# Kernel optimization log

Hardware: AMD Instinct MI355X
Metric: run time of the kernel (lower is better)

Reference implementation:

```python
import jax, jax.numpy as jnp
import numpy as np


def _conv_relu(x, w, b):
    # keras Conv2D: NHWC input, HWIO kernel, VALID padding, stride 1, relu
    y = jax.lax.conv_general_dilated(
        x, w, window_strides=(1, 1), padding='VALID',
        dimension_numbers=('NHWC', 'HWIO', 'NHWC'))
    return jax.nn.relu(y + b)


def _maxpool2(x):
    # keras MaxPooling2D((2,2)): window 2x2, stride 2, VALID
    return jax.lax.reduce_window(
        x, -jnp.inf, jax.lax.max,
        window_dimensions=(1, 2, 2, 1), window_strides=(1, 2, 2, 1),
        padding='VALID')


def setup_inputs() -> dict:
    key = jax.random.key(0)
    ks = jax.random.split(key, 8)
    B = 4096
    return {
        'x': jax.random.normal(ks[0], (B, 14, 14, 1), jnp.float32),
        'conv1_w': jax.random.normal(ks[1], (3, 3, 1, 32), jnp.float32) * 0.1,
        'conv1_b': jnp.zeros((32,), jnp.float32),
        'conv2_w': jax.random.normal(ks[2], (3, 3, 32, 64), jnp.float32) * 0.05,
        'conv2_b': jnp.zeros((64,), jnp.float32),
        # trainable grid, initialized as tf.linspace(0,1,grid_size=50)
        'grid': jnp.linspace(0.0, 1.0, 50, dtype=jnp.float32),
        # KANLayer splines: output_dim=128 weights, each (input_dim=256, grid_size=50)
        'kan1_w': jax.random.normal(ks[3], (128, 256, 50), jnp.float32) * 0.05,
        # SimplifiedKANLayer splines: output_dim=64 weights, each (input_dim=128,)
        'kan2_w': jax.random.normal(ks[4], (64, 128), jnp.float32) * 0.05,
        'dense_w': jax.random.normal(ks[5], (64, 10), jnp.float32) * 0.05,
        'dense_b': jnp.zeros((10,), jnp.float32),
    }


def reference(x, conv1_w, conv1_b, conv2_w, conv2_b, grid, kan1_w, kan2_w,
              dense_w, dense_b):
    h = _conv_relu(x, conv1_w, conv1_b)   # (B,12,12,32)
    h = _maxpool2(h)                      # (B,6,6,32)
    h = _conv_relu(h, conv2_w, conv2_b)   # (B,4,4,64)
    h = _maxpool2(h)                      # (B,2,2,64)
    B = h.shape[0]
    h = h.reshape(B, -1)                  # (B,256) keras Flatten order (H,W,C)
    # KANLayer: linear hat basis relu(1-|x-g|) per (feature,grid), contracted
    # against per-output coefficients: out[b,o] = sum_{d,g} W[o,d,g]*basis[b,d,g]
    basis = jax.nn.relu(1.0 - jnp.abs(h[:, :, None] - grid[None, None, :]))  # (B,256,50)
    h = jnp.einsum('bdg,odg->bo', basis, kan1_w)  # (B,128)
    # SimplifiedKANLayer: out[b,o] = sum_d W2[o,d]*relu(h[b,d])
    h = jnp.einsum('bd,od->bo', jax.nn.relu(h), kan2_w)  # (B,64)
    return jax.nn.softmax(h @ dense_w + dense_b, axis=-1)  # (B,10)
```

## Files before the change

### kernel.cpp

```cpp
#include <hip/hip_runtime.h>
#include <hip/hip_bf16.h>
#include <hip/hip_fp16.h>

typedef float v2f __attribute__((ext_vector_type(2)));
typedef _Float16 f16x8 __attribute__((ext_vector_type(8)));
typedef float f32x4 __attribute__((ext_vector_type(4)));

#define NBC 4

__global__ __launch_bounds__(256) void k_prep(
    const float* __restrict__ kan1_w, const float* __restrict__ w2,
    const float* __restrict__ kan2_w, __half* __restrict__ tabN,
    _Float16* __restrict__ w2f, __half2* __restrict__ w2t) {
  __shared__ float wsh[128][51];
  int bid = blockIdx.x;
  int t = threadIdx.x;
  if (bid < 1024) {
    int d = bid >> 2;
    int q = bid & 3;
#pragma unroll
    for (int i = t; i < 128 * 50; i += 256) {
      int oo = i / 50;
      int g = i - oo * 50;
      wsh[oo][g] = kan1_w[(size_t)oo * 12800 + (size_t)d * 50 + g];
    }
    __syncthreads();
    int o = t & 127;
    int jh = t >> 7;
    const float* wr = &wsh[o][0];
    __half* trow = tabN + (size_t)d * 197 * 128 + o;
    const float inv98 = 1.0f / 98.0f;
    int ci = q * 2 + jh;
    int k0 = (ci * 98) >> 3;
    int k1 = ((ci + 1) * 98) >> 3;
    float lowW = 0.f, lowG = 0.f, highW = 0.f, highG = 0.f;
    {
      int gl0 = k0 - 48 > 0 ? k0 - 48 : 0;
      int gl1 = k0 < 49 ? k0 : 49;
      for (int g = gl0; g <= gl1; ++g) {
        float w = wr[g], gg = (float)g * (1.0f / 49.0f);
        lowW += w; lowG += w * gg;
      }
      for (int g = k0 + 1; g < 50; ++g) {
        float w = wr[g], gg = (float)g * (1.0f / 49.0f);
        highW += w; highG += w * gg;
      }
    }
    for (int k = k0; k < k1; ++k) {
      float A = highW - lowW;
      float Bc = (lowW + highW) + lowG - highG;
      float c0 = (float)(2 * k) * inv98 + 0.5f * inv98;
      float c1 = c0 + inv98;
      trow[(size_t)(2 * k) * 128] = __float2half(fmaf(A, c0, Bc));
      trow[(size_t)(2 * k + 1) * 128] = __float2half(fmaf(A, c1, Bc));
      if (k + 1 <= 49) {
        float wg = wr[k + 1], gg = (float)(k + 1) * (1.0f / 49.0f);
        lowW += wg; lowG += wg * gg;
        highW -= wg; highG -= wg * gg;
      }
      if (k >= 48) {
        float wg = wr[k - 48], gg = (float)(k - 48) * (1.0f / 49.0f);
        lowW -= wg; lowG -= wg * gg;
      }
    }
    if (ci == 7) trow[(size_t)196 * 128] = __float2half(0.f);
    return;
  }
  if (bid < 1096) {
    int i = (bid - 1024) * 256 + t;
    int n = i & 63;
    int row = i >> 6;
    int ci = row & 31;
    int tap = row >> 5;
    w2f[((tap * 4 + (ci >> 3)) * 64 + n) * 8 + (ci & 7)] = (_Float16)w2[i];
    return;
  }
  {
    int i = (bid - 1096) * 256 + t;
    int dp = i >> 6;
    int o = i & 63;
    w2t[i] = __floats2half2_rn(kan2_w[o * 128 + 2 * dp],
                               kan2_w[o * 128 + 2 * dp + 1]);
  }
}

__global__ __launch_bounds__(256)
__attribute__((amdgpu_waves_per_eu(2, 4))) void k_conv(
    const float* __restrict__ x, const float* __restrict__ w1,
    const float* __restrict__ b1, const _Float16* __restrict__ w2f,
    const float* __restrict__ b2, unsigned short* __restrict__ metaG) {
  __shared__ __align__(16) char sm1[4864];
  __shared__ __align__(16) char sm2[11520];
  float* xs = (float*)sm1;
  float* w1s = xs + NBC * 224;
  float* b1s = w1s + 288;
  _Float16* h1l = (_Float16*)sm2;
  int t = threadIdx.x;
  int bid = blockIdx.x;
  int b0 = bid * NBC;
  {
    for (int i = t; i < NBC * 224; i += 256) {
      int blb = i / 224;
      int rem = i - blb * 224;
      int r = rem >> 4;
      int cc = rem & 15;
      xs[i] = (cc < 14) ? x[(size_t)(b0 + blb) * 196 + r * 14 + cc] : 0.f;
    }
    for (int i = t; i < 288; i += 256) w1s[i] = w1[i];
    if (t < 32) b1s[t] = b1[t];
  }
  __syncthreads();
  int p = t >> 6;
  int c = t & 63;
  {
    int ch = c & 31;
    int half = c >> 5;
    float wr[9];
#pragma unroll
    for (int j = 0; j < 9; ++j) wr[j] = w1s[j * 32 + ch];
    float bias = b1s[ch];
    int y0 = 3 * half;
    const float* xb = xs + p * 224;
    _Float16* hrow = h1l + p * 1440 + ch;
#pragma unroll
    for (int yy = 0; yy < 3; ++yy) {
      int y = y0 + yy;
      float xr[4][16];
#pragma unroll
      for (int r = 0; r < 4; ++r) {
        float4* dstp = (float4*)xr[r];
        const float4* srcp = (const float4*)(xb + (2 * y + r) * 16);
#pragma unroll
        for (int q = 0; q < 4; ++q) dstp[q] = srcp[q];
      }
#pragma unroll
      for (int xx = 0; xx < 6; ++xx) {
        float m = -1e30f;
#pragma unroll
        for (int py = 0; py < 2; ++py)
#pragma unroll
          for (int px = 0; px < 2; ++px) {
            float s = 0.f;
#pragma unroll
            for (int dy = 0; dy < 3; ++dy)
#pragma unroll
              for (int dx = 0; dx < 3; ++dx)
                s = fmaf(xr[py + dy][2 * xx + px + dx], wr[dy * 3 + dx], s);
            m = fmaxf(m, s);
          }
        hrow[(y * 6 + xx) * 40] = (_Float16)fmaxf(m + bias, 0.f);
      }
    }
  }
  __syncthreads();
  {
    int lm = c & 15;
    int lk = c >> 4;
    int mbase = (lm >> 2) * 6 + (lm & 3);
    f32x4 acc[4];
#pragma unroll
    for (int nt = 0; nt < 4; ++nt) acc[nt] = (f32x4){0.f, 0.f, 0.f, 0.f};
    const _Float16* h0 = &h1l[p * 1440 + lk * 8];
#pragma unroll
    for (int tap = 0; tap < 9; ++tap) {
      int tapoff = (tap / 3) * 6 + (tap % 3);
      int po = (mbase + tapoff) * 40;
      f16x8 a0 = *(const f16x8*)(h0 + po);
      const _Float16* wb = &w2f[((tap * 4 + lk) * 64 + lm) * 8];
      f16x8 bf0 = *(const f16x8*)(wb);
      f16x8 bf1 = *(const f16x8*)(wb + 128);
      f16x8 bf2 = *(const f16x8*)(wb + 256);
      f16x8 bf3 = *(const f16x8*)(wb + 384);
      acc[0] = __builtin_amdgcn_mfma_f32_16x16x32_f16(a0, bf0, acc[0], 0, 0, 0);
      acc[1] = __builtin_amdgcn_mfma_f32_16x16x32_f16(a0, bf1, acc[1], 0, 0, 0);
      acc[2] = __builtin_amdgcn_mfma_f32_16x16x32_f16(a0, bf2, acc[2], 0, 0, 0);
      acc[3] = __builtin_amdgcn_mfma_f32_16x16x32_f16(a0, bf3, acc[3], 0, 0, 0);
    }
    float bias[4];
#pragma unroll
    for (int nt = 0; nt < 4; ++nt) bias[nt] = b2[nt * 16 + lm];
#pragma unroll
    for (int nt = 0; nt < 4; ++nt) {
      f32x4 A = acc[nt];
      float m01 = fmaxf(A.x, A.y);
      float m23 = fmaxf(A.z, A.w);
      m01 = fmaxf(m01, __shfl_xor(m01, 16));
      m23 = fmaxf(m23, __shfl_xor(m23, 16));
      float val = (lk & 1) ? m23 : m01;
      val = fmaxf(val + bias[nt], 0.f);
      int d = lk * 64 + nt * 16 + lm;
      int k = (int)(val * 98.0f);
      k = k > 196 ? 196 : k;
      metaG[(size_t)(b0 + p) * 256 + d] = (unsigned short)(d * 197 + k);
    }
  }
}

__global__ __launch_bounds__(256) void k_gather(
    const __half* __restrict__ tabN, const unsigned short* __restrict__ metaG,
    float* __restrict__ partialG, int B) {
  __shared__ unsigned short ms[32][32];
  int bid = blockIdx.x;
  int t = threadIdx.x;
  int s = bid & 7;
  int gid = bid >> 3;
  int b0 = gid * 32;
  {
    unsigned int* mdst = (unsigned int*)&ms[0][0];
    for (int j = t; j < 512; j += 256) {
      int row = j >> 4, col = j & 15;
      mdst[j] = *(const unsigned int*)(metaG + (size_t)(b0 + row) * 256 +
                                       s * 32 + col * 2);
    }
  }
  __syncthreads();
  int w = t >> 6;
  int l = t & 63;
  for (int bb = 0; bb < 8; ++bb) {
    int brow = w * 8 + bb;
    float ax = 0.f, ay = 0.f;
#pragma unroll
    for (int ch = 0; ch < 4; ++ch) {
      __half2 hsum = __builtin_bit_cast(__half2, 0u);
#pragma unroll
      for (int dd = 0; dd < 8; ++dd) {
        int off = ((int)ms[brow][ch * 8 + dd]) << 7;
        hsum = __hadd2(hsum, *(const __half2*)(tabN + off + 2 * l));
      }
      float2 f = __half22float2(hsum);
      ax += f.x;
      ay += f.y;
    }
    *(float2*)(partialG + ((size_t)s * B + (b0 + brow)) * 128 + 2 * l) =
        make_float2(ax, ay);
  }
}

__global__ __launch_bounds__(256) void k_tail(
    const float* __restrict__ partialG, const __half2* __restrict__ w2t,
    const float* __restrict__ dense_w, const float* __restrict__ dense_b,
    float* __restrict__ out, int B) {
  __shared__ float vs[NBC * 128];
  __shared__ float us[NBC * 64];
  __shared__ float ls[NBC * 12];
  int t = threadIdx.x;
  int bid = blockIdx.x;
  int b0 = bid * NBC;
  for (int i = t; i < NBC * 128; i += 256) {
    int bb = i >> 7;
    int o = i & 127;
    float sum = 0.f;
#pragma unroll
    for (int s = 0; s < 8; ++s)
      sum += partialG[((size_t)s * B + (b0 + bb)) * 128 + o];
    vs[i] = fmaxf(sum, 0.f);
  }
  __syncthreads();
  int p = t >> 6;
  int c = t & 63;
  {
    float a = 0.f;
    const float* v0 = vs + p * 128;
#pragma unroll 8
    for (int dp = 0; dp < 64; ++dp) {
      float2 wf = __half22float2(w2t[dp * 64 + c]);
      float2 vq = *(const float2*)(v0 + 2 * dp);
      a = fmaf(wf.x, vq.x, a);
      a = fmaf(wf.y, vq.y, a);
    }
    us[p * 64 + c] = a;
  }
  __syncthreads();
  if (t < NBC * 10) {
    int b = t / 10;
    int j = t - b * 10;
    float s = dense_b[j];
    for (int k2 = 0; k2 < 64; ++k2)
      s = fmaf(us[b * 64 + k2], dense_w[k2 * 10 + j], s);
    ls[b * 12 + j] = s;
  }
  __syncthreads();
  if (t < NBC) {
    int b = t;
    float m = -1e30f;
#pragma unroll
    for (int j = 0; j < 10; ++j) m = fmaxf(m, ls[b * 12 + j]);
    float e[10];
    float sum = 0.f;
#pragma unroll
    for (int j = 0; j < 10; ++j) {
      e[j] = __expf(ls[b * 12 + j] - m);
      sum += e[j];
    }
    float inv = 1.0f / sum;
#pragma unroll
    for (int j = 0; j < 10; ++j) out[(size_t)(b0 + b) * 10 + j] = e[j] * inv;
  }
}

extern "C" void kernel_launch(void* const* d_in, const int* in_sizes, int n_in,
                              void* d_out, int out_size, void* d_ws, size_t ws_size,
                              hipStream_t stream) {
  const float* x      = (const float*)d_in[0];
  const float* w1     = (const float*)d_in[1];
  const float* b1     = (const float*)d_in[2];
  const float* w2     = (const float*)d_in[3];
  const float* b2     = (const float*)d_in[4];
  const float* kan1_w = (const float*)d_in[6];
  const float* kan2_w = (const float*)d_in[7];
  const float* dw     = (const float*)d_in[8];
  const float* db     = (const float*)d_in[9];
  float* out = (float*)d_out;
  int B = in_sizes[0] / 196;

  char* wsb = (char*)d_ws;
  __half* tabN = (__half*)wsb;
  size_t off1 = (size_t)256 * 197 * 128 * sizeof(__half);
  off1 = (off1 + 255) & ~(size_t)255;
  _Float16* w2f = (_Float16*)(wsb + off1);
  size_t off2 = off1 + 18432 * sizeof(_Float16);
  off2 = (off2 + 255) & ~(size_t)255;
  __half2* w2t = (__half2*)(wsb + off2);
  size_t off3 = off2 + 4096 * sizeof(__half2);
  off3 = (off3 + 255) & ~(size_t)255;
  unsigned short* metaG = (unsigned short*)(wsb + off3);
  size_t off4 = off3 + (size_t)B * 256 * sizeof(unsigned short);
  off4 = (off4 + 255) & ~(size_t)255;
  float* partialG = (float*)(wsb + off4);

  k_prep<<<dim3(1112), dim3(256), 0, stream>>>(kan1_w, w2, kan2_w, tabN, w2f, w2t);
  k_conv<<<dim3(B / NBC), dim3(256), 0, stream>>>(x, w1, b1, w2f, b2, metaG);
  k_gather<<<dim3(8 * (B / 32)), dim3(256), 0, stream>>>(tabN, metaG, partialG, B);
  k_tail<<<dim3(B / NBC), dim3(256), 0, stream>>>(partialG, w2t, dw, db, out, B);
}
```

Baseline: 124.4 us.

## Replace KAN1 table-gather with dense MFMA contraction over hat basis

Drops the precomputed piecewise-linear lookup table and gather kernel, and computes the KAN layer as a dense fp16 MFMA GEMM. The hat basis is generated on the fly from conv outputs stored as fp16, against kan1_w repacked to a padded (256x56) K layout. This removes the large table build and the scattered gathers, but adds a roughly 14336-long K reduction per output. The split-K partials also drop from 8 to 4. The prep kernel now only converts weights, and k_kan1 launches 256 blocks with one block per CU.

```diff
diff --git a/kernel.cpp b/kernel.cpp
--- a/kernel.cpp
+++ b/kernel.cpp
@@ -10,64 +10,22 @@
 
 __global__ __launch_bounds__(256) void k_prep(
     const float* __restrict__ kan1_w, const float* __restrict__ w2,
-    const float* __restrict__ kan2_w, __half* __restrict__ tabN,
+    const float* __restrict__ kan2_w, _Float16* __restrict__ w1f,
     _Float16* __restrict__ w2f, __half2* __restrict__ w2t) {
-  __shared__ float wsh[128][51];
   int bid = blockIdx.x;
   int t = threadIdx.x;
-  if (bid < 1024) {
-    int d = bid >> 2;
-    int q = bid & 3;
-#pragma unroll
-    for (int i = t; i < 128 * 50; i += 256) {
-      int oo = i / 50;
-      int g = i - oo * 50;
-      wsh[oo][g] = kan1_w[(size_t)oo * 12800 + (size_t)d * 50 + g];
-    }
-    __syncthreads();
-    int o = t & 127;
-    int jh = t >> 7;
-    const float* wr = &wsh[o][0];
-    __half* trow = tabN + (size_t)d * 197 * 128 + o;
-    const float inv98 = 1.0f / 98.0f;
-    int ci = q * 2 + jh;
-    int k0 = (ci * 98) >> 3;
-    int k1 = ((ci + 1) * 98) >> 3;
-    float lowW = 0.f, lowG = 0.f, highW = 0.f, highG = 0.f;
-    {
-      int gl0 = k0 - 48 > 0 ? k0 - 48 : 0;
-      int gl1 = k0 < 49 ? k0 : 49;
-      for (int g = gl0; g <= gl1; ++g) {
-        float w = wr[g], gg = (float)g * (1.0f / 49.0f);
-        lowW += w; lowG += w * gg;
-      }
-      for (int g = k0 + 1; g < 50; ++g) {
-        float w = wr[g], gg = (float)g * (1.0f / 49.0f);
-        highW += w; highG += w * gg;
-      }
-    }
-    for (int k = k0; k < k1; ++k) {
-      float A = highW - lowW;
-      float Bc = (lowW + highW) + lowG - highG;
-      float c0 = (float)(2 * k) * inv98 + 0.5f * inv98;
-      float c1 = c0 + inv98;
-      trow[(size_t)(2 * k) * 128] = __float2half(fmaf(A, c0, Bc));
-      trow[(size_t)(2 * k + 1) * 128] = __float2half(fmaf(A, c1, Bc));
-      if (k + 1 <= 49) {
-        float wg = wr[k + 1], gg = (float)(k + 1) * (1.0f / 49.0f);
-        lowW += wg; lowG += wg * gg;
-        highW -= wg; highG -= wg * gg;
-      }
-      if (k >= 48) {
-        float wg = wr[k - 48], gg = (float)(k - 48) * (1.0f / 49.0f);
-        lowW -= wg; lowG -= wg * gg;
-      }
-    }
-    if (ci == 7) trow[(size_t)196 * 128] = __float2half(0.f);
+  if (bid < 7168) {
+    int i = bid * 256 + t;
+    int o = i / 14336;
+    int kk = i - o * 14336;
+    int d = kk / 56;
+    int g = kk - d * 56;
+    float val = (g < 50) ? kan1_w[(size_t)o * 12800 + d * 50 + g] : 0.f;
+    w1f[(size_t)(kk >> 3) * 1024 + o * 8 + (kk & 7)] = (_Float16)val;
     return;
   }
-  if (bid < 1096) {
-    int i = (bid - 1024) * 256 + t;
+  if (bid < 7240) {
+    int i = (bid - 7168) * 256 + t;
     int n = i & 63;
     int row = i >> 6;
     int ci = row & 31;
@@ -76,7 +34,7 @@
     return;
   }
   {
-    int i = (bid - 1096) * 256 + t;
+    int i = (bid - 7240) * 256 + t;
     int dp = i >> 6;
     int o = i & 63;
     w2t[i] = __floats2half2_rn(kan2_w[o * 128 + 2 * dp],
@@ -88,7 +46,7 @@
 __attribute__((amdgpu_waves_per_eu(2, 4))) void k_conv(
     const float* __restrict__ x, const float* __restrict__ w1,
     const float* __restrict__ b1, const _Float16* __restrict__ w2f,
-    const float* __restrict__ b2, unsigned short* __restrict__ metaG) {
+    const float* __restrict__ b2, __half* __restrict__ hG) {
   __shared__ __align__(16) char sm1[4864];
   __shared__ __align__(16) char sm2[11520];
   float* xs = (float*)sm1;
@@ -189,51 +147,65 @@
       float val = (lk & 1) ? m23 : m01;
       val = fmaxf(val + bias[nt], 0.f);
       int d = lk * 64 + nt * 16 + lm;
-      int k = (int)(val * 98.0f);
-      k = k > 196 ? 196 : k;
-      metaG[(size_t)(b0 + p) * 256 + d] = (unsigned short)(d * 197 + k);
-    }
-  }
-}
-
-__global__ __launch_bounds__(256) void k_gather(
-    const __half* __restrict__ tabN, const unsigned short* __restrict__ metaG,
-    float* __restrict__ partialG, int B) {
-  __shared__ unsigned short ms[32][32];
+      hG[(size_t)(b0 + p) * 256 + d] = __float2half(val);
+    }
+  }
+}
+
+__global__ __launch_bounds__(256, 1) void k_kan1(
+    const __half* __restrict__ hG, const _Float16* __restrict__ w1f,
+    float* __restrict__ partial, int B) {
+  __shared__ _Float16 hl[64][72];
   int bid = blockIdx.x;
   int t = threadIdx.x;
-  int s = bid & 7;
-  int gid = bid >> 3;
-  int b0 = gid * 32;
-  {
-    unsigned int* mdst = (unsigned int*)&ms[0][0];
-    for (int j = t; j < 512; j += 256) {
-      int row = j >> 4, col = j & 15;
-      mdst[j] = *(const unsigned int*)(metaG + (size_t)(b0 + row) * 256 +
-                                       s * 32 + col * 2);
-    }
+  int mt = bid >> 2;
+  int kq = bid & 3;
+  int b0 = mt * 64;
+#pragma unroll
+  for (int j = t; j < 512; j += 256) {
+    int row = j >> 3, c8 = j & 7;
+    *(f16x8*)&hl[row][c8 * 8] =
+        *(const f16x8*)(hG + (size_t)(b0 + row) * 256 + kq * 64 + c8 * 8);
   }
   __syncthreads();
   int w = t >> 6;
-  int l = t & 63;
-  for (int bb = 0; bb < 8; ++bb) {
-    int brow = w * 8 + bb;
-    float ax = 0.f, ay = 0.f;
-#pragma unroll
-    for (int ch = 0; ch < 4; ++ch) {
-      __half2 hsum = __builtin_bit_cast(__half2, 0u);
-#pragma unroll
-      for (int dd = 0; dd < 8; ++dd) {
-        int off = ((int)ms[brow][ch * 8 + dd]) << 7;
-        hsum = __hadd2(hsum, *(const __half2*)(tabN + off + 2 * l));
-      }
-      float2 f = __half22float2(hsum);
-      ax += f.x;
-      ay += f.y;
-    }
-    *(float2*)(partialG + ((size_t)s * B + (b0 + brow)) * 128 + 2 * l) =
-        make_float2(ax, ay);
-  }
+  int lane = t & 63;
+  int m = lane & 15;
+  int kg = lane >> 4;
+  const _Float16* hrow = &hl[w * 16 + m][0];
+  f32x4 acc[8];
+#pragma unroll
+  for (int nt = 0; nt < 8; ++nt) acc[nt] = (f32x4){0.f, 0.f, 0.f, 0.f};
+  const _Float16* wbase = w1f + ((size_t)kq * 448 + kg) * 1024 + m * 8;
+  for (int ks = 0; ks < 112; ++ks) {
+    const _Float16* wp = wbase + (size_t)ks * 4096;
+    f16x8 bf[8];
+#pragma unroll
+    for (int nt = 0; nt < 8; ++nt) bf[nt] = *(const f16x8*)(wp + nt * 128);
+    int xx = ks * 4 + kg;
+    int dl = (xx * 9363) >> 16;
+    int xr = xx - 7 * dl;
+    float h = (float)hrow[dl];
+    float t0 = h - (float)(xr * 8) * (1.0f / 49.0f);
+    f16x8 af;
+#pragma unroll
+    for (int j = 0; j < 8; ++j) {
+      float b = 1.0f - __builtin_fabsf(t0 - (float)j * (1.0f / 49.0f));
+      af[j] = (_Float16)fmaxf(b, 0.f);
+    }
+#pragma unroll
+    for (int nt = 0; nt < 8; ++nt)
+      acc[nt] =
+          __builtin_amdgcn_mfma_f32_16x16x32_f16(af, bf[nt], acc[nt], 0, 0, 0);
+  }
+  float* pb = partial + ((size_t)kq * B + b0 + w * 16) * 128;
+#pragma unroll
+  for (int nt = 0; nt < 8; ++nt)
+#pragma unroll
+    for (int ri = 0; ri < 4; ++ri) {
+      int r = kg * 4 + ri;
+      pb[(size_t)r * 128 + nt * 16 + m] = acc[nt][ri];
+    }
 }
 
 __global__ __launch_bounds__(256) void k_tail(
@@ -251,7 +223,7 @@
     int o = i & 127;
     float sum = 0.f;
 #pragma unroll
-    for (int s = 0; s < 8; ++s)
+    for (int s = 0; s < 4; ++s)
       sum += partialG[((size_t)s * B + (b0 + bb)) * 128 + o];
     vs[i] = fmaxf(sum, 0.f);
   }
@@ -314,8 +286,8 @@
   int B = in_sizes[0] / 196;
 
   char* wsb = (char*)d_ws;
-  __half* tabN = (__half*)wsb;
-  size_t off1 = (size_t)256 * 197 * 128 * sizeof(__half);
+  _Float16* w1f = (_Float16*)wsb;
+  size_t off1 = (size_t)14336 * 128 * sizeof(_Float16);
   off1 = (off1 + 255) & ~(size_t)255;
   _Float16* w2f = (_Float16*)(wsb + off1);
   size_t off2 = off1 + 18432 * sizeof(_Float16);
@@ -323,13 +295,13 @@
   __half2* w2t = (__half2*)(wsb + off2);
   size_t off3 = off2 + 4096 * sizeof(__half2);
   off3 = (off3 + 255) & ~(size_t)255;
-  unsigned short* metaG = (unsigned short*)(wsb + off3);
-  size_t off4 = off3 + (size_t)B * 256 * sizeof(unsigned short);
+  __half* hG = (__half*)(wsb + off3);
+  size_t off4 = off3 + (size_t)B * 256 * sizeof(__half);
   off4 = (off4 + 255) & ~(size_t)255;
   float* partialG = (float*)(wsb + off4);
 
-  k_prep<<<dim3(1112), dim3(256), 0, stream>>>(kan1_w, w2, kan2_w, tabN, w2f, w2t);
-  k_conv<<<dim3(B / NBC), dim3(256), 0, stream>>>(x, w1, b1, w2f, b2, metaG);
-  k_gather<<<dim3(8 * (B / 32)), dim3(256), 0, stream>>>(tabN, metaG, partialG, B);
+  k_prep<<<dim3(7256), dim3(256), 0, stream>>>(kan1_w, w2, kan2_w, w1f, w2f, w2t);
+  k_conv<<<dim3(B / NBC), dim3(256), 0, stream>>>(x, w1, b1, w2f, b2, hG);
+  k_kan1<<<dim3(256), dim3(256), 0, stream>>>(hG, w1f, partialG, B);
   k_tail<<<dim3(B / NBC), dim3(256), 0, stream>>>(partialG, w2t, dw, db, out, B);
 }
```

New measurement: 141.7 us. 13.9% more time.
